# Kernel optimization log

Hardware: AMD Instinct MI355X
Metric: run time of the kernel (lower is better)

The kernel has to match this reference:

```python
import jax, jax.numpy as jnp
import numpy as np

B, T, E, H, A, V, C = 4, 256, 256, 256, 256, 32000, 100
NEG = -1e9


def setup_inputs() -> dict:
    key = jax.random.key(0)
    cnt = [0]
    def nk():
        cnt[0] += 1
        return jax.random.fold_in(key, cnt[0])
    def rn(shape, scale=0.05):
        return jax.random.normal(nk(), shape, jnp.float32) * scale
    inp = {
        'input_ids': jax.random.randint(nk(), (B, T), 0, V),
        'category_ids': jax.random.randint(nk(), (B, T), 0, C),
        'emb': rn((V, E)),
        'cat_emb': rn((C, E)),
    }
    in_sizes = [2 * E, H]
    for li, ins in enumerate(in_sizes):
        inp[f'Wih{li}'] = rn((ins, 3 * H)); inp[f'bih{li}'] = rn((3 * H,))
        inp[f'Whh{li}'] = rn((H, 3 * H)); inp[f'bhh{li}'] = rn((3 * H,))
        inp[f'Wh{li}'] = rn((H, A));      inp[f'bh{li}'] = rn((A,))
        inp[f'Wx{li}'] = rn((ins, A));    inp[f'bx{li}'] = rn((A,))
        inp[f'Wth{li}'] = rn((H, A));     inp[f'bth{li}'] = rn((A,))
        inp[f'v{li}'] = rn((A,));         inp[f'bv{li}'] = rn((1,))
    inp['Wctx'] = rn((H + E, 500)); inp['bctx'] = rn((500,))
    inp['Wout'] = rn((500, V));     inp['bout'] = rn((V,))
    return inp


def _cell(x, h, tape, t, Wih, bih, Whh, bhh, Wh, bh, Wx, bx, Wth, bth, v, bv):
    # attention over memory tape positions j < t (tape rows >= t are zeros, masked out)
    att = jnp.tanh(tape @ Wh + bh + (x @ Wx + bx)[:, None, :] + (h @ Wth + bth)[:, None, :])  # [B,T,A]
    scores = att @ v + bv  # [B,T]
    mask = jnp.arange(tape.shape[1]) < t
    scores = jnp.where(mask[None, :], scores, NEG)
    w = jax.nn.softmax(scores, axis=1)
    agg = jnp.einsum('bt,bth->bh', w, tape)
    agg = jnp.where(t > 0, agg, h)  # empty tape at t=0 -> use hidden directly
    gi = x @ Wih + bih
    gh = agg @ Whh + bhh
    ir, iu, inew = jnp.split(gi, 3, axis=1)
    hr, hu, hn = jnp.split(gh, 3, axis=1)
    r = jax.nn.sigmoid(ir + hr)
    u = jax.nn.sigmoid(iu + hu)
    n = jnp.tanh(inew + r * hn)
    return (1.0 - u) * n + u * agg


def _forward(input_ids, category_ids, emb, cat_emb, p0, p1, Wctx, bctx, Wout, bout):
    we = emb[input_ids]          # [B,T,E]
    ce = cat_emb[category_ids]   # [B,T,E]
    x_seq = jnp.concatenate([we, ce], axis=-1)  # [B,T,2E]

    def step(carry, xs):
        h0, h1, tape0, tape1 = carry
        x_t, c_t, t = xs
        # layer 0: category added to both embedding halves
        li0 = jax.nn.relu(x_t + jnp.tile(c_t, (1, 2)))
        nh0 = _cell(li0, h0, tape0, t, *p0)
        tape0 = tape0.at[:, t].set(nh0)
        # layer 1 (dropout is identity in eval)
        li1 = jax.nn.relu(nh0 + c_t)
        nh1 = _cell(li1, h1, tape1, t, *p1)
        tape1 = tape1.at[:, t].set(nh1)
        ctx = jnp.tanh(jnp.concatenate([nh1, c_t], axis=-1) @ Wctx + bctx)
        logits = ctx @ Wout + bout
        return (nh0, nh1, tape0, tape1), logits

    Bn = input_ids.shape[0]
    init = (jnp.zeros((Bn, H), jnp.float32), jnp.zeros((Bn, H), jnp.float32),
            jnp.zeros((Bn, T, H), jnp.float32), jnp.zeros((Bn, T, H), jnp.float32))
    xs = (jnp.swapaxes(x_seq, 0, 1), jnp.swapaxes(ce, 0, 1), jnp.arange(T))
    (h0, h1, _, _), outs = jax.lax.scan(jax.checkpoint(step), init, xs)
    return jnp.swapaxes(outs, 0, 1), h0, h1


def reference(input_ids, category_ids, emb, cat_emb,
              Wih0, bih0, Whh0, bhh0, Wh0, bh0, Wx0, bx0, Wth0, bth0, v0, bv0,
              Wih1, bih1, Whh1, bhh1, Wh1, bh1, Wx1, bx1, Wth1, bth1, v1, bv1,
              Wctx, bctx, Wout, bout):
    p0 = (Wih0, bih0, Whh0, bhh0, Wh0, bh0, Wx0, bx0, Wth0, bth0, v0, bv0)
    p1 = (Wih1, bih1, Whh1, bhh1, Wh1, bh1, Wx1, bx1, Wth1, bth1, v1, bv1)
    return _forward(input_ids, category_ids, emb, cat_emb, p0, p1, Wctx, bctx, Wout, bout)
```

## Files before the change

### kernel.cpp

```cpp
#include <hip/hip_runtime.h>

#define DEVINL __device__ __forceinline__

constexpr int kB = 4, kT = 256, kH = 256, kA = 256, kV = 32000;
constexpr int NBLKS = 128;
constexpr int NGRP = 32;
constexpr int NTHR = 512;
constexpr int WSL = 8;
constexpr int SBIAS = 1 << 24;
constexpr int SBIAS_TOT = NGRP * SBIAS;
constexpr unsigned long long CANARY = ~0ull;

typedef __attribute__((ext_vector_type(8))) short bf16x8;
typedef __attribute__((ext_vector_type(4))) float f32x4;

DEVINL float fexp2(float x) { float y; asm("v_exp_f32 %0, %1" : "=v"(y) : "v"(x)); return y; }
DEVINL float frcp(float x)  { float y; asm("v_rcp_f32 %0, %1" : "=v"(y) : "v"(x)); return y; }
DEVINL float f_tanh(float x) {
  float t = fexp2(x * 2.88539008f);
  return 1.f - 2.f * frcp(t + 1.f);
}
DEVINL float f_sig(float x) { return frcp(1.f + fexp2(-x * 1.44269504f)); }

DEVINL float bfu2f(unsigned short u) {
  union { unsigned int i; float f; } c; c.i = ((unsigned int)u) << 16; return c.f;
}
DEVINL unsigned short f2bfu(float f) {
  union { float f; unsigned int i; } c; c.f = f;
  unsigned int r = c.i + 0x7fffu + ((c.i >> 16) & 1u);
  return (unsigned short)(r >> 16);
}
DEVINL unsigned int f2u(float f) { union { float f; unsigned int i; } c; c.f = f; return c.i; }
DEVINL float u2f(unsigned int u) { union { unsigned int i; float f; } c; c.i = u; return c.f; }

DEVINL unsigned long long aload64(const unsigned long long* p) {
  return __hip_atomic_load(p, __ATOMIC_RELAXED, __HIP_MEMORY_SCOPE_AGENT);
}
DEVINL void astore64(unsigned long long* p, unsigned long long v) {
  __hip_atomic_store(p, v, __ATOMIC_RELAXED, __HIP_MEMORY_SCOPE_AGENT);
}

DEVINL bool sready(unsigned long long v) {
  unsigned int lo = (unsigned int)v, hi = (unsigned int)(v >> 32);
  return (((lo + (1u << 23)) >> 24) == (unsigned)NGRP) &&
         (((hi + (1u << 23)) >> 24) == (unsigned)NGRP);
}

DEVINL float dot_bf64s(const float* x, const unsigned short* w, int q) {
  float a0 = 0.f, a1 = 0.f, a2 = 0.f, a3 = 0.f;
  const float4*  x4 = (const float4*)x;
  const ushort4* w4 = (const ushort4*)w;
#pragma unroll
  for (int i = 0; i < 16; ++i) {
    int c = q + 4 * i;
    float4 xv = x4[c]; ushort4 wv = w4[c];
    a0 += xv.x * bfu2f(wv.x);
    a1 += xv.y * bfu2f(wv.y);
    a2 += xv.z * bfu2f(wv.z);
    a3 += xv.w * bfu2f(wv.w);
  }
  return (a0 + a1) + (a2 + a3);
}

DEVINL float sc4(const unsigned short* p4p, const float* xp, const float* vr) {
  ushort4 p4 = *(const ushort4*)p4p;
  float accA, accB;
  accA  = f_tanh(bfu2f(p4.x) + xp[0]) * vr[0];
  accB  = f_tanh(bfu2f(p4.y) + xp[1]) * vr[1];
  accA += f_tanh(bfu2f(p4.z) + xp[2]) * vr[2];
  accB += f_tanh(bfu2f(p4.w) + xp[3]) * vr[3];
  return accA + accB;
}

__global__ void init_kernel(int* dst, int nz, int val) {
  for (int i = blockIdx.x * blockDim.x + threadIdx.x; i < nz; i += gridDim.x * blockDim.x)
    dst[i] = val;
}

__global__ void embed_kernel(const int* __restrict__ ids, const int* __restrict__ cids,
                             const float* __restrict__ emb, const float* __restrict__ cat_emb,
                             float* __restrict__ li0_all, float* __restrict__ ce_all,
                             float* __restrict__ cat1_all) {
  int bt = blockIdx.x, e = threadIdx.x;
  int id = ids[bt], cid = cids[bt];
  float we = emb[id * kH + e];
  float ce = cat_emb[cid * kH + e];
  li0_all[bt * 512 + e]       = fmaxf(we + ce, 0.f);
  li0_all[bt * 512 + 256 + e] = fmaxf(ce + ce, 0.f);
  ce_all[bt * 256 + e] = ce;
  cat1_all[bt * 512 + 256 + e] = ce;
}

__global__ __launch_bounds__(256) void gemm_f32(const float* __restrict__ A,
                                                const float* __restrict__ Wm,
                                                const float* __restrict__ bias,
                                                float* __restrict__ C,
                                                int M, int N, int K) {
  __shared__ __align__(16) float As[16][68];
  __shared__ __align__(16) float Bs[16][68];
  int tid = threadIdx.x;
  int tx = tid & 15, ty = tid >> 4;
  int row0 = blockIdx.y * 64, col0 = blockIdx.x * 64;
  int ar = tid >> 2;
  int ak = (tid & 3) * 4;
  int br = tid >> 4;
  int bc = (tid & 15) * 4;
  float acc[4][4] = {};
  for (int k0 = 0; k0 < K; k0 += 16) {
    float4 av = {0.f, 0.f, 0.f, 0.f};
    if (k0 + ak < K) av = *(const float4*)(A + (size_t)(row0 + ar) * K + k0 + ak);
    As[ak + 0][ar] = av.x; As[ak + 1][ar] = av.y; As[ak + 2][ar] = av.z; As[ak + 3][ar] = av.w;
    float4 bv = {0.f, 0.f, 0.f, 0.f};
    int wrow = k0 + br;
    if (wrow < K) {
      if (col0 + bc + 3 < N) bv = *(const float4*)(Wm + (size_t)wrow * N + col0 + bc);
      else {
        float t[4] = {0.f, 0.f, 0.f, 0.f};
        for (int u = 0; u < 4; ++u) if (col0 + bc + u < N) t[u] = Wm[(size_t)wrow * N + col0 + bc + u];
        bv.x = t[0]; bv.y = t[1]; bv.z = t[2]; bv.w = t[3];
      }
    }
    *(float4*)&Bs[br][bc] = bv;
    __syncthreads();
#pragma unroll
    for (int kk = 0; kk < 16; ++kk) {
      float4 a4 = *(const float4*)&As[kk][ty * 4];
      float4 b4 = *(const float4*)&Bs[kk][tx * 4];
      acc[0][0] += a4.x * b4.x; acc[0][1] += a4.x * b4.y; acc[0][2] += a4.x * b4.z; acc[0][3] += a4.x * b4.w;
      acc[1][0] += a4.y * b4.x; acc[1][1] += a4.y * b4.y; acc[1][2] += a4.y * b4.z; acc[1][3] += a4.y * b4.w;
      acc[2][0] += a4.z * b4.x; acc[2][1] += a4.z * b4.y; acc[2][2] += a4.z * b4.z; acc[2][3] += a4.z * b4.w;
      acc[3][0] += a4.w * b4.x; acc[3][1] += a4.w * b4.y; acc[3][2] += a4.w * b4.z; acc[3][3] += a4.w * b4.w;
    }
    __syncthreads();
  }
#pragma unroll
  for (int i = 0; i < 4; ++i) {
    int r = row0 + ty * 4 + i;
#pragma unroll
    for (int j = 0; j < 4; ++j) {
      int c = col0 + tx * 4 + j;
      if (c < N) C[(size_t)r * N + c] = acc[i][j] + bias[c];
    }
  }
}

__global__ __launch_bounds__(256) void gemm_ctx_bf16(const float* __restrict__ A,
                                                     const float* __restrict__ Wm,
                                                     const float* __restrict__ bias,
                                                     unsigned short* __restrict__ Cb) {
  const int N = 500, K = 512;
  __shared__ __align__(16) float As[16][68];
  __shared__ __align__(16) float Bs[16][68];
  int tid = threadIdx.x;
  int tx = tid & 15, ty = tid >> 4;
  int row0 = blockIdx.y * 64, col0 = blockIdx.x * 64;
  int ar = tid >> 2;
  int ak = (tid & 3) * 4;
  int br = tid >> 4;
  int bc = (tid & 15) * 4;
  float acc[4][4] = {};
  for (int k0 = 0; k0 < K; k0 += 16) {
    float4 av = *(const float4*)(A + (size_t)(row0 + ar) * K + k0 + ak);
    As[ak + 0][ar] = av.x; As[ak + 1][ar] = av.y; As[ak + 2][ar] = av.z; As[ak + 3][ar] = av.w;
    float4 bv = {0.f, 0.f, 0.f, 0.f};
    int wrow = k0 + br;
    if (col0 + bc + 3 < N) bv = *(const float4*)(Wm + (size_t)wrow * N + col0 + bc);
    else {
      float t[4] = {0.f, 0.f, 0.f, 0.f};
      for (int u = 0; u < 4; ++u) if (col0 + bc + u < N) t[u] = Wm[(size_t)wrow * N + col0 + bc + u];
      bv.x = t[0]; bv.y = t[1]; bv.z = t[2]; bv.w = t[3];
    }
    *(float4*)&Bs[br][bc] = bv;
    __syncthreads();
#pragma unroll
    for (int kk = 0; kk < 16; ++kk) {
      float4 a4 = *(const float4*)&As[kk][ty * 4];
      float4 b4 = *(const float4*)&Bs[kk][tx * 4];
      acc[0][0] += a4.x * b4.x; acc[0][1] += a4.x * b4.y; acc[0][2] += a4.x * b4.z; acc[0][3] += a4.x * b4.w;
      acc[1][0] += a4.y * b4.x; acc[1][1] += a4.y * b4.y; acc[1][2] += a4.y * b4.z; acc[1][3] += a4.y * b4.w;
      acc[2][0] += a4.z * b4.x; acc[2][1] += a4.z * b4.y; acc[2][2] += a4.z * b4.z; acc[2][3] += a4.z * b4.w;
      acc[3][0] += a4.w * b4.x; acc[3][1] += a4.w * b4.y; acc[3][2] += a4.w * b4.z; acc[3][3] += a4.w * b4.w;
    }
    __syncthreads();
  }
#pragma unroll
  for (int i = 0; i < 4; ++i) {
    int r = row0 + ty * 4 + i;
#pragma unroll
    for (int j = 0; j < 4; ++j) {
      int c = col0 + tx * 4 + j;
      if (c < N) {
        float v = f_tanh(acc[i][j] + bias[c]);
        Cb[(size_t)r * 512 + c] = f2bfu(v);
      } else {
        Cb[(size_t)r * 512 + c] = 0;
      }
    }
  }
}

__global__ __launch_bounds__(256) void gemm_logits_mfma(
    const unsigned short* __restrict__ A,
    const float* __restrict__ Wout,
    const float* __restrict__ bout,
    float* __restrict__ C) {
  __shared__ __align__(16) unsigned short Bt[64][520];
  const int tid = threadIdx.x;
  const int n0 = blockIdx.x * 64;

  for (int idx = tid; idx < 512 * 16; idx += 256) {
    int k = idx >> 4, nq = (idx & 15) << 2;
    if (k < 500) {
      float4 v = *(const float4*)(Wout + (size_t)k * 32000 + n0 + nq);
      Bt[nq + 0][k] = f2bfu(v.x); Bt[nq + 1][k] = f2bfu(v.y);
      Bt[nq + 2][k] = f2bfu(v.z); Bt[nq + 3][k] = f2bfu(v.w);
    } else {
      Bt[nq + 0][k] = 0; Bt[nq + 1][k] = 0; Bt[nq + 2][k] = 0; Bt[nq + 3][k] = 0;
    }
  }
  __syncthreads();

  const int l = tid & 63, w = tid >> 6;
  const int lrow = l & 15, lk = (l >> 4) * 8;
  float bia0 = bout[n0 +  0 + lrow];
  float bia1 = bout[n0 + 16 + lrow];
  float bia2 = bout[n0 + 32 + lrow];
  float bia3 = bout[n0 + 48 + lrow];

  for (int m0 = 0; m0 < 1024; m0 += 64) {
    f32x4 acc0 = {0.f, 0.f, 0.f, 0.f}, acc1 = acc0, acc2 = acc0, acc3 = acc0;
    const unsigned short* Arow = A + (size_t)(m0 + w * 16 + lrow) * 512 + lk;
#pragma unroll
    for (int ks = 0; ks < 16; ++ks) {
      bf16x8 a  = *(const bf16x8*)(Arow + ks * 32);
      bf16x8 b0 = *(const bf16x8*)&Bt[ 0 + lrow][ks * 32 + lk];
      bf16x8 b1 = *(const bf16x8*)&Bt[16 + lrow][ks * 32 + lk];
      bf16x8 b2 = *(const bf16x8*)&Bt[32 + lrow][ks * 32 + lk];
      bf16x8 b3 = *(const bf16x8*)&Bt[48 + lrow][ks * 32 + lk];
      acc0 = __builtin_amdgcn_mfma_f32_16x16x32_bf16(a, b0, acc0, 0, 0, 0);
      acc1 = __builtin_amdgcn_mfma_f32_16x16x32_bf16(a, b1, acc1, 0, 0, 0);
      acc2 = __builtin_amdgcn_mfma_f32_16x16x32_bf16(a, b2, acc2, 0, 0, 0);
      acc3 = __builtin_amdgcn_mfma_f32_16x16x32_bf16(a, b3, acc3, 0, 0, 0);
    }
    int orow = m0 + w * 16 + (l >> 4) * 4;
#pragma unroll
    for (int r = 0; r < 4; ++r) {
      float* Cr = C + (size_t)(orow + r) * 32000 + n0;
      Cr[ 0 + lrow] = acc0[r] + bia0;
      Cr[16 + lrow] = acc1[r] + bia1;
      Cr[32 + lrow] = acc2[r] + bia2;
      Cr[48 + lrow] = acc3[r] + bia3;
    }
  }
}

__global__ __launch_bounds__(NTHR, 1) void coop_kernel(
    const float* __restrict__ gi0_all, const float* __restrict__ xw0_all,
    const float* __restrict__ ce_all,
    unsigned long long* __restrict__ nh0p, unsigned long long* __restrict__ nh1p,
    float* __restrict__ cat1_all, float* __restrict__ out_tail,
    unsigned long long* __restrict__ s0buf, unsigned long long* __restrict__ s1buf,
    const float* __restrict__ Whh0, const float* __restrict__ bhh0,
    const float* __restrict__ Wh0, const float* __restrict__ bh0,
    const float* __restrict__ Wth0, const float* __restrict__ bth0,
    const float* __restrict__ v0,
    const float* __restrict__ Wih1, const float* __restrict__ bih1,
    const float* __restrict__ Whh1, const float* __restrict__ bhh1,
    const float* __restrict__ Wh1, const float* __restrict__ bh1,
    const float* __restrict__ Wx1, const float* __restrict__ bx1,
    const float* __restrict__ Wth1, const float* __restrict__ bth1,
    const float* __restrict__ v1) {
  __shared__ __align__(16) unsigned short tWhh0_s[kT][24];
  __shared__ __align__(16) unsigned short tWhh1_s[kT][24];
  __shared__ __align__(16) unsigned short tape0_s[kT][8];
  __shared__ __align__(16) unsigned short tape1_s[kT][8];
  __shared__ __align__(16) unsigned short tWh0_s[kT][8];
  __shared__ __align__(16) unsigned short tWh1_s[kT][8];
  __shared__ __align__(16) unsigned short Wh0c[WSL][264], Wth0c[WSL][264];
  __shared__ __align__(16) unsigned short Wh1c[WSL][264], Wth1c[WSL][264], Wx1c[WSL][264];
  __shared__ __align__(16) unsigned short Whh0c[24][264], Whh1c[24][264], Wih1c[24][264];
  __shared__ float bh0s[8], bth0s[8], bh1s[8], bth1s[8], bx1s[8];
  __shared__ float bhh0s[24], bhh1s[24], bih1s[24];
  __shared__ __align__(16) float nh0_s[260], nh1_s[260], li1_s[260];
  __shared__ __align__(16) float sm_s[2][260];
  __shared__ float xps0_s[8], xps1a_s[8], xps1b_s[8];
  __shared__ float gi1_s[24], gh0_s[24], gh1_s[24];
  __shared__ float agg0_s[8], agg1_s[8], redsum_s[2][2];
  __shared__ float gipre_s[3][8];
  __shared__ float v0s[8], v1s[8];

  const int bid = blockIdx.x, tid = threadIdx.x;
  const int grp = bid >> 5;
  const int bidg = bid & 31;
  const int c0 = bidg * WSL;
  const int gb = grp;
  unsigned long long* S0 = s0buf + grp * 384;
  unsigned long long* S1 = s1buf + grp * 384;

  for (int idx = tid; idx < WSL * kH; idx += NTHR) {
    int c = idx >> 8, h = idx & 255, col = c0 + c;
    Wh0c[c][h]  = f2bfu(Wh0[h * kA + col]);
    Wth0c[c][h] = f2bfu(Wth0[h * kA + col]);
    Wh1c[c][h]  = f2bfu(Wh1[h * kA + col]);
    Wth1c[c][h] = f2bfu(Wth1[h * kA + col]);
    Wx1c[c][h]  = f2bfu(Wx1[h * kA + col]);
  }
  for (int idx = tid; idx < 24 * kH; idx += NTHR) {
    int cc = idx >> 8, h = idx & 255;
    int n = (cc >> 3) * kH + c0 + (cc & 7);
    Whh0c[cc][h] = f2bfu(Whh0[h * 768 + n]);
    Whh1c[cc][h] = f2bfu(Whh1[h * 768 + n]);
    Wih1c[cc][h] = f2bfu(Wih1[h * 768 + n]);
  }
  if (tid < 8) {
    int c = c0 + tid;
    bh0s[tid] = bh0[c]; bth0s[tid] = bth0[c];
    bh1s[tid] = bh1[c]; bth1s[tid] = bth1[c]; bx1s[tid] = bx1[c];
    v0s[tid] = v0[c]; v1s[tid] = v1[c];
  }
  if (tid < 24) {
    int n = (tid >> 3) * kH + c0 + (tid & 7);
    bhh0s[tid] = bhh0[n]; bhh1s[tid] = bhh1[n]; bih1s[tid] = bih1[n];
  }
  __syncthreads();

  if (tid < 8) {
    int c = tid, hcol = c0 + c;
    const float* gi = gi0_all + (size_t)(gb * kT) * 768;
    float r = f_sig(gi[hcol] + bhh0s[c]);
    float u = f_sig(gi[256 + hcol] + bhh0s[8 + c]);
    float n = f_tanh(gi[512 + hcol] + r * bhh0s[16 + c]);
    float val = (1.f - u) * n;
    tape0_s[0][c] = f2bfu(val);
    float other = __shfl_xor(val, 1);
    if ((c & 1) == 0) {
      unsigned long long pk = (unsigned long long)f2u(val) |
                              ((unsigned long long)f2u(other) << 32);
      astore64(&nh0p[(size_t)(gb * kT) * 128 + bidg * 4 + (c >> 1)], pk);
    }
  }

  const float SCL = 65536.f;
  const float fxi = 1.44269504f / 65536.f;

  for (int k = 0; k < kT; ++k) {
    if (tid < 256) {
      int which = tid >> 7;
      int pr = tid & 127, h = pr * 2;
      if (which == 0) {
        const unsigned long long* p = &nh0p[(size_t)(gb * kT + k) * 128 + pr];
        unsigned long long v = aload64(p);
        int it = 0;
        while (v == CANARY) {
          v = aload64(p);
          if (++it > (1 << 24)) break;
        }
        float lo = u2f((unsigned int)v), hi = u2f((unsigned int)(v >> 32));
        nh0_s[h] = lo; nh0_s[h + 1] = hi;
        float2 ce2 = *(const float2*)&ce_all[(size_t)(gb * kT + k) * 256 + h];
        li1_s[h]     = fmaxf(lo + ce2.x, 0.f);
        li1_s[h + 1] = fmaxf(hi + ce2.y, 0.f);
      } else if (k > 0) {
        const unsigned long long* p = &nh1p[(size_t)(gb * kT + k - 1) * 128 + pr];
        unsigned long long v = aload64(p);
        int it = 0;
        while (v == CANARY) {
          v = aload64(p);
          if (++it > (1 << 24)) break;
        }
        nh1_s[h]     = u2f((unsigned int)v);
        nh1_s[h + 1] = u2f((unsigned int)(v >> 32));
      }
    }
    if (tid >= 256 && tid < 264 && k < kT - 1) {
      int c = tid - 256, hcol = c0 + c;
      const float* gi = gi0_all + (size_t)(gb * kT + k + 1) * 768;
      gipre_s[0][c] = gi[hcol];
      gipre_s[1][c] = gi[256 + hcol];
      gipre_s[2][c] = gi[512 + hcol];
    }
    if (tid >= NTHR - 8) {
      int z = tid - (NTHR - 8);
      int pz = (k + 1) % 3;
      int idx = bidg * 4 + (z & 3);
      if (z < 4) astore64(&S0[pz * 128 + idx], 0ull);
      else       astore64(&S1[pz * 128 + idx], 0ull);
    }
    __syncthreads();

    {
      int p = tid >> 2, q = tid & 3;
      if (p < 40) {
        if (k < kT - 1) {
          if (p < 8) {
            int c = p;
            float acc = dot_bf64s(nh0_s, Wth0c[c], q);
            acc += __shfl_xor(acc, 1); acc += __shfl_xor(acc, 2);
            if (q == 0) {
              float xw = xw0_all[(size_t)(gb * kT + k + 1) * kA + c0 + c];
              xps0_s[c] = acc + bth0s[c] + xw;
            }
          } else if (p < 16) {
            int c = p - 8;
            float acc = dot_bf64s(nh0_s, Wh0c[c], q);
            acc += __shfl_xor(acc, 1); acc += __shfl_xor(acc, 2);
            if (q == 0) tWh0_s[k][c] = f2bfu(acc + bh0s[c]);
          } else {
            int cc = p - 16;
            float acc = dot_bf64s(nh0_s, Whh0c[cc], q);
            acc += __shfl_xor(acc, 1); acc += __shfl_xor(acc, 2);
            if (q == 0) tWhh0_s[k][cc] = f2bfu(acc);
          }
        }
      } else if (p < 72) {
        if (p < 64) {
          int cc = p - 40;
          float acc = dot_bf64s(li1_s, Wih1c[cc], q);
          acc += __shfl_xor(acc, 1); acc += __shfl_xor(acc, 2);
          if (q == 0) gi1_s[cc] = acc + bih1s[cc];
        } else {
          int c = p - 64;
          float acc = dot_bf64s(li1_s, Wx1c[c], q);
          acc += __shfl_xor(acc, 1); acc += __shfl_xor(acc, 2);
          if (q == 0) xps1a_s[c] = acc + bx1s[c];
        }
      } else if (p < 112) {
        if (k > 0) {
          if (p < 80) {
            int c = p - 72;
            float acc = dot_bf64s(nh1_s, Wth1c[c], q);
            acc += __shfl_xor(acc, 1); acc += __shfl_xor(acc, 2);
            if (q == 0) xps1b_s[c] = acc + bth1s[c];
          } else if (p < 88) {
            int c = p - 80;
            float acc = dot_bf64s(nh1_s, Wh1c[c], q);
            acc += __shfl_xor(acc, 1); acc += __shfl_xor(acc, 2);
            if (q == 0) tWh1_s[k - 1][c] = f2bfu(acc + bh1s[c]);
          } else {
            int cc = p - 88;
            float acc = dot_bf64s(nh1_s, Whh1c[cc], q);
            acc += __shfl_xor(acc, 1); acc += __shfl_xor(acc, 2);
            if (q == 0) tWhh1_s[k - 1][cc] = f2bfu(acc);
          }
        }
      }
    }
    __syncthreads();

    {
      int cnt0w = k + 1, cnt1w = k;
      int np0 = (k < kT - 1) ? ((cnt0w + 1) >> 1) : 0;
      int np1 = (cnt1w + 1) >> 1;
      int pk = k % 3;
      unsigned long long* d0 = S0 + pk * 128;
      unsigned long long* d1 = S1 + pk * 128;
      for (int pp = tid; pp < np0 + np1; pp += NTHR) {
        float p0, p1; unsigned long long* dst;
        if (pp < np0) {
          int j0 = 2 * pp;
          p0 = sc4(&tWh0_s[j0][0], xps0_s, v0s) + sc4(&tWh0_s[j0][4], xps0_s + 4, v0s + 4);
          p1 = 0.f;
          if (j0 + 1 < cnt0w)
            p1 = sc4(&tWh0_s[j0 + 1][0], xps0_s, v0s) + sc4(&tWh0_s[j0 + 1][4], xps0_s + 4, v0s + 4);
          dst = d0 + pp;
        } else {
          int pr = pp - np0, j0 = 2 * pr;
          float xp[8];
#pragma unroll
          for (int c = 0; c < 8; ++c) xp[c] = xps1a_s[c] + xps1b_s[c];
          p0 = sc4(&tWh1_s[j0][0], xp, v1s) + sc4(&tWh1_s[j0][4], xp + 4, v1s + 4);
          p1 = 0.f;
          if (j0 + 1 < cnt1w)
            p1 = sc4(&tWh1_s[j0 + 1][0], xp, v1s) + sc4(&tWh1_s[j0 + 1][4], xp + 4, v1s + 4);
          dst = d1 + pr;
        }
        int q0 = (int)rintf(p0 * SCL) + SBIAS;
        int q1 = (int)rintf(p1 * SCL) + SBIAS;
        unsigned long long add = (unsigned long long)(unsigned int)q0 |
                                 ((unsigned long long)(unsigned int)q1 << 32);
        __hip_atomic_fetch_add(dst, add, __ATOMIC_RELAXED, __HIP_MEMORY_SCOPE_AGENT);
      }
    }
    __syncthreads();

    int cnt0 = (k < kT - 1) ? (k + 1) : 0;
    int cnt1 = k;
    if (tid < 256) {
      int r = tid >> 7, lane = tid & 127;
      float sum = 0.f;
      int cnt = (r == 0) ? cnt0 : cnt1;
      if (cnt) {
        int pk = k % 3;
        const unsigned long long* sb = (r == 0) ? S0 + pk * 128 : S1 + pk * 128;
        int npr = (cnt + 1) >> 1;
        if (lane < npr) {
          unsigned long long v = aload64(&sb[lane]);
          int it = 0;
          while (!sready(v)) {
            v = aload64(&sb[lane]);
            if (++it > (1 << 24)) break;
          }
          int lo = (int)(unsigned int)(v & 0xffffffffull) - SBIAS_TOT;
          int hi = (int)(unsigned int)(v >> 32) - SBIAS_TOT;
          float e0 = fexp2((float)lo * fxi);
          sm_s[r][2 * lane] = e0; sum += e0;
          if (2 * lane + 1 < cnt) {
            float e1 = fexp2((float)hi * fxi);
            sm_s[r][2 * lane + 1] = e1; sum += e1;
          }
        }
      }
      for (int m = 32; m >= 1; m >>= 1) sum += __shfl_xor(sum, m);
      if ((tid & 63) == 0) redsum_s[r][(tid >> 6) & 1] = sum;
    }
    __syncthreads();

    {
      int slot = tid >> 3, sub = tid & 7;
      float accA = 0.f, accB = 0.f;
      if (slot < 24) {
        if (cnt0) {
          int cc = slot;
#pragma unroll 4
          for (int j = sub; j < cnt0; j += 16) accA += sm_s[0][j] * bfu2f(tWhh0_s[j][cc]);
#pragma unroll 4
          for (int j = sub + 8; j < cnt0; j += 16) accB += sm_s[0][j] * bfu2f(tWhh0_s[j][cc]);
          float acc = accA + accB;
          acc += __shfl_xor(acc, 1); acc += __shfl_xor(acc, 2); acc += __shfl_xor(acc, 4);
          if (sub == 0) gh0_s[cc] = acc * frcp(redsum_s[0][0] + redsum_s[0][1]) + bhh0s[cc];
        }
      } else if (slot < 32) {
        if (cnt0) {
          int c = slot - 24;
#pragma unroll 4
          for (int j = sub; j < cnt0; j += 16) accA += sm_s[0][j] * bfu2f(tape0_s[j][c]);
#pragma unroll 4
          for (int j = sub + 8; j < cnt0; j += 16) accB += sm_s[0][j] * bfu2f(tape0_s[j][c]);
          float acc = accA + accB;
          acc += __shfl_xor(acc, 1); acc += __shfl_xor(acc, 2); acc += __shfl_xor(acc, 4);
          if (sub == 0) agg0_s[c] = acc * frcp(redsum_s[0][0] + redsum_s[0][1]);
        }
      } else if (slot < 56) {
        if (cnt1) {
          int cc = slot - 32;
#pragma unroll 4
          for (int j = sub; j < cnt1; j += 16) accA += sm_s[1][j] * bfu2f(tWhh1_s[j][cc]);
#pragma unroll 4
          for (int j = sub + 8; j < cnt1; j += 16) accB += sm_s[1][j] * bfu2f(tWhh1_s[j][cc]);
          float acc = accA + accB;
          acc += __shfl_xor(acc, 1); acc += __shfl_xor(acc, 2); acc += __shfl_xor(acc, 4);
          if (sub == 0) gh1_s[cc] = acc * frcp(redsum_s[1][0] + redsum_s[1][1]) + bhh1s[cc];
        }
      } else if (slot < 64) {
        if (cnt1) {
          int c = slot - 56;
#pragma unroll 4
          for (int j = sub; j < cnt1; j += 16) accA += sm_s[1][j] * bfu2f(tape1_s[j][c]);
#pragma unroll 4
          for (int j = sub + 8; j < cnt1; j += 16) accB += sm_s[1][j] * bfu2f(tape1_s[j][c]);
          float acc = accA + accB;
          acc += __shfl_xor(acc, 1); acc += __shfl_xor(acc, 2); acc += __shfl_xor(acc, 4);
          if (sub == 0) agg1_s[c] = acc * frcp(redsum_s[1][0] + redsum_s[1][1]);
        }
      }
    }
    __syncthreads();

    if (tid < 8) {
      if (k < kT - 1) {
        int c = tid, hcol = c0 + c, t0 = k + 1;
        float agg = agg0_s[c];
        float r = f_sig(gipre_s[0][c] + gh0_s[c]);
        float u = f_sig(gipre_s[1][c] + gh0_s[8 + c]);
        float n = f_tanh(gipre_s[2][c] + r * gh0_s[16 + c]);
        float val = (1.f - u) * n + u * agg;
        tape0_s[t0][c] = f2bfu(val);
        if (t0 == kT - 1) out_tail[gb * kH + hcol] = val;
        float other = __shfl_xor(val, 1);
        if ((c & 1) == 0) {
          unsigned long long pk = (unsigned long long)f2u(val) |
                                  ((unsigned long long)f2u(other) << 32);
          astore64(&nh0p[(size_t)(gb * kT + t0) * 128 + bidg * 4 + (c >> 1)], pk);
        }
      }
    } else if (tid >= 64 && tid < 72) {
      int c = tid - 64, hcol = c0 + c;
      float ghr, ghu, ghn, agg;
      if (k > 0) { ghr = gh1_s[c]; ghu = gh1_s[8 + c]; ghn = gh1_s[16 + c]; agg = agg1_s[c]; }
      else       { ghr = bhh1s[c]; ghu = bhh1s[8 + c]; ghn = bhh1s[16 + c]; agg = 0.f; }
      float r = f_sig(gi1_s[c] + ghr);
      float u = f_sig(gi1_s[8 + c] + ghu);
      float n = f_tanh(gi1_s[16 + c] + r * ghn);
      float val = (1.f - u) * n + u * agg;
      tape1_s[k][c] = f2bfu(val);
      cat1_all[(size_t)(gb * kT + k) * 512 + hcol] = val;
      if (k == kT - 1) out_tail[kB * kH + gb * kH + hcol] = val;
      float other = __shfl_xor(val, 1);
      if ((c & 1) == 0) {
        unsigned long long pk = (unsigned long long)f2u(val) |
                                ((unsigned long long)f2u(other) << 32);
        astore64(&nh1p[(size_t)(gb * kT + k) * 128 + bidg * 4 + (c >> 1)], pk);
      }
    }
  }
}

extern "C" void kernel_launch(void* const* d_in, const int* in_sizes, int n_in,
                              void* d_out, int out_size, void* d_ws, size_t ws_size,
                              hipStream_t stream) {
  const int*   input_ids    = (const int*)d_in[0];
  const int*   category_ids = (const int*)d_in[1];
  const float* emb     = (const float*)d_in[2];
  const float* cat_emb = (const float*)d_in[3];
  const float* Wih0 = (const float*)d_in[4];
  const float* bih0 = (const float*)d_in[5];
  const float* Whh0 = (const float*)d_in[6];  const float* bhh0 = (const float*)d_in[7];
  const float* Wh0  = (const float*)d_in[8];  const float* bh0  = (const float*)d_in[9];
  const float* Wx0  = (const float*)d_in[10]; const float* bx0  = (const float*)d_in[11];
  const float* Wth0 = (const float*)d_in[12]; const float* bth0 = (const float*)d_in[13];
  const float* v0   = (const float*)d_in[14];
  const float* Wih1 = (const float*)d_in[16]; const float* bih1 = (const float*)d_in[17];
  const float* Whh1 = (const float*)d_in[18]; const float* bhh1 = (const float*)d_in[19];
  const float* Wh1  = (const float*)d_in[20]; const float* bh1  = (const float*)d_in[21];
  const float* Wx1  = (const float*)d_in[22]; const float* bx1  = (const float*)d_in[23];
  const float* Wth1 = (const float*)d_in[24]; const float* bth1 = (const float*)d_in[25];
  const float* v1   = (const float*)d_in[26];
  const float* Wctx = (const float*)d_in[28]; const float* bctx = (const float*)d_in[29];
  const float* Wout = (const float*)d_in[30]; const float* bout = (const float*)d_in[31];

  float* ws = (float*)d_ws;
  float* li0_all  = ws;
  float* ce_all   = li0_all + 524288;
  float* gi0_all  = ce_all + 262144;
  float* xw0_all  = gi0_all + 786432;
  unsigned long long* nh0p = (unsigned long long*)(xw0_all + 262144);
  unsigned long long* nh1p = nh0p + 131072;
  float* cat1_all = (float*)(nh1p + 131072);
  unsigned short* ctx_bf = (unsigned short*)(cat1_all + 524288);

  unsigned long long* s0buf = (unsigned long long*)li0_all;
  unsigned long long* s1buf = s0buf + 1536;
  int    nzero_s  = 2 * 1536 * 2;
  int    nfill_nh = 2 * 131072 * 2;

  float* out = (float*)d_out;
  float* out_tail = out + (size_t)kB * kT * kV;

  embed_kernel<<<dim3(kB * kT), dim3(256), 0, stream>>>(input_ids, category_ids, emb, cat_emb,
                                                        li0_all, ce_all, cat1_all);
  gemm_f32<<<dim3(12, 16), dim3(256), 0, stream>>>(li0_all, Wih0, bih0, gi0_all, 1024, 768, 512);
  gemm_f32<<<dim3(4, 16), dim3(256), 0, stream>>>(li0_all, Wx0, bx0, xw0_all, 1024, 256, 512);
  init_kernel<<<dim3(8), dim3(512), 0, stream>>>((int*)s0buf, nzero_s, 0);
  init_kernel<<<dim3(128), dim3(512), 0, stream>>>((int*)nh0p, nfill_nh, -1);
  coop_kernel<<<dim3(NBLKS), dim3(NTHR), 0, stream>>>(gi0_all, xw0_all, ce_all, nh0p, nh1p,
      cat1_all, out_tail, s0buf, s1buf,
      Whh0, bhh0, Wh0, bh0, Wth0, bth0, v0,
      Wih1, bih1, Whh1, bhh1, Wh1, bh1, Wx1, bx1, Wth1, bth1, v1);
  gemm_ctx_bf16<<<dim3(8, 16), dim3(256), 0, stream>>>(cat1_all, Wctx, bctx, ctx_bf);
  gemm_logits_mfma<<<dim3(500), dim3(256), 0, stream>>>(ctx_bf, Wout, bout, out);
}
```

Baseline: 2.055 ms.

## Use bf16 MFMA for input projections and overlap nh1 wait with its dot products

```diff
diff --git a/kernel.cpp b/kernel.cpp
--- a/kernel.cpp
+++ b/kernel.cpp
@@ -62,6 +62,27 @@
   return (a0 + a1) + (a2 + a3);
 }
 
+DEVINL float dot_nh1g(const unsigned long long* xrow, const unsigned short* w, int q) {
+  float a0 = 0.f, a1 = 0.f, a2 = 0.f, a3 = 0.f;
+  const ushort4* w4 = (const ushort4*)w;
+#pragma unroll
+  for (int i = 0; i < 16; ++i) {
+    int c = q + 4 * i;
+    unsigned long long va = aload64(xrow + 2 * c);
+    int it = 0;
+    while (va == CANARY) { va = aload64(xrow + 2 * c); if (++it > (1 << 24)) break; }
+    unsigned long long vb = aload64(xrow + 2 * c + 1);
+    it = 0;
+    while (vb == CANARY) { vb = aload64(xrow + 2 * c + 1); if (++it > (1 << 24)) break; }
+    ushort4 wv = w4[c];
+    a0 += u2f((unsigned int)va)         * bfu2f(wv.x);
+    a1 += u2f((unsigned int)(va >> 32)) * bfu2f(wv.y);
+    a2 += u2f((unsigned int)vb)         * bfu2f(wv.z);
+    a3 += u2f((unsigned int)(vb >> 32)) * bfu2f(wv.w);
+  }
+  return (a0 + a1) + (a2 + a3);
+}
+
 DEVINL float sc4(const unsigned short* p4p, const float* xp, const float* vr) {
   ushort4 p4 = *(const ushort4*)p4p;
   float accA, accB;
@@ -79,68 +100,64 @@
 
 __global__ void embed_kernel(const int* __restrict__ ids, const int* __restrict__ cids,
                              const float* __restrict__ emb, const float* __restrict__ cat_emb,
-                             float* __restrict__ li0_all, float* __restrict__ ce_all,
+                             unsigned short* __restrict__ li0bf, float* __restrict__ ce_all,
                              float* __restrict__ cat1_all) {
   int bt = blockIdx.x, e = threadIdx.x;
   int id = ids[bt], cid = cids[bt];
   float we = emb[id * kH + e];
   float ce = cat_emb[cid * kH + e];
-  li0_all[bt * 512 + e]       = fmaxf(we + ce, 0.f);
-  li0_all[bt * 512 + 256 + e] = fmaxf(ce + ce, 0.f);
+  li0bf[bt * 512 + e]       = f2bfu(fmaxf(we + ce, 0.f));
+  li0bf[bt * 512 + 256 + e] = f2bfu(fmaxf(ce + ce, 0.f));
   ce_all[bt * 256 + e] = ce;
   cat1_all[bt * 512 + 256 + e] = ce;
 }
 
-__global__ __launch_bounds__(256) void gemm_f32(const float* __restrict__ A,
-                                                const float* __restrict__ Wm,
-                                                const float* __restrict__ bias,
-                                                float* __restrict__ C,
-                                                int M, int N, int K) {
-  __shared__ __align__(16) float As[16][68];
-  __shared__ __align__(16) float Bs[16][68];
-  int tid = threadIdx.x;
-  int tx = tid & 15, ty = tid >> 4;
-  int row0 = blockIdx.y * 64, col0 = blockIdx.x * 64;
-  int ar = tid >> 2;
-  int ak = (tid & 3) * 4;
-  int br = tid >> 4;
-  int bc = (tid & 15) * 4;
-  float acc[4][4] = {};
-  for (int k0 = 0; k0 < K; k0 += 16) {
-    float4 av = {0.f, 0.f, 0.f, 0.f};
-    if (k0 + ak < K) av = *(const float4*)(A + (size_t)(row0 + ar) * K + k0 + ak);
-    As[ak + 0][ar] = av.x; As[ak + 1][ar] = av.y; As[ak + 2][ar] = av.z; As[ak + 3][ar] = av.w;
-    float4 bv = {0.f, 0.f, 0.f, 0.f};
-    int wrow = k0 + br;
-    if (wrow < K) {
-      if (col0 + bc + 3 < N) bv = *(const float4*)(Wm + (size_t)wrow * N + col0 + bc);
-      else {
-        float t[4] = {0.f, 0.f, 0.f, 0.f};
-        for (int u = 0; u < 4; ++u) if (col0 + bc + u < N) t[u] = Wm[(size_t)wrow * N + col0 + bc + u];
-        bv.x = t[0]; bv.y = t[1]; bv.z = t[2]; bv.w = t[3];
-      }
-    }
-    *(float4*)&Bs[br][bc] = bv;
-    __syncthreads();
-#pragma unroll
-    for (int kk = 0; kk < 16; ++kk) {
-      float4 a4 = *(const float4*)&As[kk][ty * 4];
-      float4 b4 = *(const float4*)&Bs[kk][tx * 4];
-      acc[0][0] += a4.x * b4.x; acc[0][1] += a4.x * b4.y; acc[0][2] += a4.x * b4.z; acc[0][3] += a4.x * b4.w;
-      acc[1][0] += a4.y * b4.x; acc[1][1] += a4.y * b4.y; acc[1][2] += a4.y * b4.z; acc[1][3] += a4.y * b4.w;
-      acc[2][0] += a4.z * b4.x; acc[2][1] += a4.z * b4.y; acc[2][2] += a4.z * b4.z; acc[2][3] += a4.z * b4.w;
-      acc[3][0] += a4.w * b4.x; acc[3][1] += a4.w * b4.y; acc[3][2] += a4.w * b4.z; acc[3][3] += a4.w * b4.w;
-    }
-    __syncthreads();
-  }
-#pragma unroll
-  for (int i = 0; i < 4; ++i) {
-    int r = row0 + ty * 4 + i;
-#pragma unroll
-    for (int j = 0; j < 4; ++j) {
-      int c = col0 + tx * 4 + j;
-      if (c < N) C[(size_t)r * N + c] = acc[i][j] + bias[c];
-    }
+__global__ __launch_bounds__(256) void gemm_mfma_f32out(
+    const unsigned short* __restrict__ A,
+    const float* __restrict__ Wm,
+    const float* __restrict__ bias,
+    float* __restrict__ C, int N) {
+  __shared__ __align__(16) unsigned short Bt[64][520];
+  const int tid = threadIdx.x;
+  const int n0 = blockIdx.x * 64, m0 = blockIdx.y * 64;
+
+  for (int idx = tid; idx < 512 * 16; idx += 256) {
+    int k = idx >> 4, nq = (idx & 15) << 2;
+    float4 v = *(const float4*)(Wm + (size_t)k * N + n0 + nq);
+    Bt[nq + 0][k] = f2bfu(v.x); Bt[nq + 1][k] = f2bfu(v.y);
+    Bt[nq + 2][k] = f2bfu(v.z); Bt[nq + 3][k] = f2bfu(v.w);
+  }
+  __syncthreads();
+
+  const int l = tid & 63, w = tid >> 6;
+  const int lrow = l & 15, lk = (l >> 4) * 8;
+  float bia0 = bias[n0 +  0 + lrow];
+  float bia1 = bias[n0 + 16 + lrow];
+  float bia2 = bias[n0 + 32 + lrow];
+  float bia3 = bias[n0 + 48 + lrow];
+
+  f32x4 acc0 = {0.f, 0.f, 0.f, 0.f}, acc1 = acc0, acc2 = acc0, acc3 = acc0;
+  const unsigned short* Arow = A + (size_t)(m0 + w * 16 + lrow) * 512 + lk;
+#pragma unroll
+  for (int ks = 0; ks < 16; ++ks) {
+    bf16x8 a  = *(const bf16x8*)(Arow + ks * 32);
+    bf16x8 b0 = *(const bf16x8*)&Bt[ 0 + lrow][ks * 32 + lk];
+    bf16x8 b1 = *(const bf16x8*)&Bt[16 + lrow][ks * 32 + lk];
+    bf16x8 b2 = *(const bf16x8*)&Bt[32 + lrow][ks * 32 + lk];
+    bf16x8 b3 = *(const bf16x8*)&Bt[48 + lrow][ks * 32 + lk];
+    acc0 = __builtin_amdgcn_mfma_f32_16x16x32_bf16(a, b0, acc0, 0, 0, 0);
+    acc1 = __builtin_amdgcn_mfma_f32_16x16x32_bf16(a, b1, acc1, 0, 0, 0);
+    acc2 = __builtin_amdgcn_mfma_f32_16x16x32_bf16(a, b2, acc2, 0, 0, 0);
+    acc3 = __builtin_amdgcn_mfma_f32_16x16x32_bf16(a, b3, acc3, 0, 0, 0);
+  }
+  int orow = m0 + w * 16 + (l >> 4) * 4;
+#pragma unroll
+  for (int r = 0; r < 4; ++r) {
+    float* Cr = C + (size_t)(orow + r) * N + n0;
+    Cr[ 0 + lrow] = acc0[r] + bia0;
+    Cr[16 + lrow] = acc1[r] + bia1;
+    Cr[32 + lrow] = acc2[r] + bia2;
+    Cr[48 + lrow] = acc3[r] + bia3;
   }
 }
 
@@ -281,7 +298,7 @@
   __shared__ __align__(16) unsigned short Whh0c[24][264], Whh1c[24][264], Wih1c[24][264];
   __shared__ float bh0s[8], bth0s[8], bh1s[8], bth1s[8], bx1s[8];
   __shared__ float bhh0s[24], bhh1s[24], bih1s[24];
-  __shared__ __align__(16) float nh0_s[260], nh1_s[260], li1_s[260];
+  __shared__ __align__(16) float nh0_s[260], li1_s[260];
   __shared__ __align__(16) float sm_s[2][260];
   __shared__ float xps0_s[8], xps1a_s[8], xps1b_s[8];
   __shared__ float gi1_s[24], gh0_s[24], gh1_s[24];
@@ -344,40 +361,48 @@
   const float fxi = 1.44269504f / 65536.f;
 
   for (int k = 0; k < kT; ++k) {
-    if (tid < 256) {
-      int which = tid >> 7;
-      int pr = tid & 127, h = pr * 2;
-      if (which == 0) {
-        const unsigned long long* p = &nh0p[(size_t)(gb * kT + k) * 128 + pr];
-        unsigned long long v = aload64(p);
-        int it = 0;
-        while (v == CANARY) {
-          v = aload64(p);
-          if (++it > (1 << 24)) break;
-        }
-        float lo = u2f((unsigned int)v), hi = u2f((unsigned int)(v >> 32));
-        nh0_s[h] = lo; nh0_s[h + 1] = hi;
-        float2 ce2 = *(const float2*)&ce_all[(size_t)(gb * kT + k) * 256 + h];
-        li1_s[h]     = fmaxf(lo + ce2.x, 0.f);
-        li1_s[h + 1] = fmaxf(hi + ce2.y, 0.f);
-      } else if (k > 0) {
-        const unsigned long long* p = &nh1p[(size_t)(gb * kT + k - 1) * 128 + pr];
-        unsigned long long v = aload64(p);
-        int it = 0;
-        while (v == CANARY) {
-          v = aload64(p);
-          if (++it > (1 << 24)) break;
-        }
-        nh1_s[h]     = u2f((unsigned int)v);
-        nh1_s[h + 1] = u2f((unsigned int)(v >> 32));
-      }
-    }
-    if (tid >= 256 && tid < 264 && k < kT - 1) {
-      int c = tid - 256, hcol = c0 + c;
-      const float* gi = gi0_all + (size_t)(gb * kT + k + 1) * 768;
-      gipre_s[0][c] = gi[hcol];
-      gipre_s[1][c] = gi[256 + hcol];
-      gipre_s[2][c] = gi[512 + hcol];
+    if (tid < 128) {
+      int pr = tid, h = pr * 2;
+      const unsigned long long* p = &nh0p[(size_t)(gb * kT + k) * 128 + pr];
+      unsigned long long v = aload64(p);
+      int it = 0;
+      while (v == CANARY) {
+        v = aload64(p);
+        if (++it > (1 << 24)) break;
+      }
+      float lo = u2f((unsigned int)v), hi = u2f((unsigned int)(v >> 32));
+      nh0_s[h] = lo; nh0_s[h + 1] = hi;
+      float2 ce2 = *(const float2*)&ce_all[(size_t)(gb * kT + k) * 256 + h];
+      li1_s[h]     = fmaxf(lo + ce2.x, 0.f);
+      li1_s[h + 1] = fmaxf(hi + ce2.y, 0.f);
+    } else if (tid < 288) {
+      if (k > 0) {
+        int p = (tid - 128) >> 2, q = tid & 3;
+        const unsigned long long* xrow = &nh1p[(size_t)(gb * kT + k - 1) * 128];
+        if (p < 8) {
+          float acc = dot_nh1g(xrow, Wth1c[p], q);
+          acc += __shfl_xor(acc, 1); acc += __shfl_xor(acc, 2);
+          if (q == 0) xps1b_s[p] = acc + bth1s[p];
+        } else if (p < 16) {
+          int c = p - 8;
+          float acc = dot_nh1g(xrow, Wh1c[c], q);
+          acc += __shfl_xor(acc, 1); acc += __shfl_xor(acc, 2);
+          if (q == 0) tWh1_s[k - 1][c] = f2bfu(acc + bh1s[c]);
+        } else {
+          int cc = p - 16;
+          float acc = dot_nh1g(xrow, Whh1c[cc], q);
+          acc += __shfl_xor(acc, 1); acc += __shfl_xor(acc, 2);
+          if (q == 0) tWhh1_s[k - 1][cc] = f2bfu(acc);
+        }
+      }
+    } else if (tid < 296) {
+      if (k < kT - 1) {
+        int c = tid - 288, hcol = c0 + c;
+        const float* gi = gi0_all + (size_t)(gb * kT + k + 1) * 768;
+        gipre_s[0][c] = gi[hcol];
+        gipre_s[1][c] = gi[256 + hcol];
+        gipre_s[2][c] = gi[512 + hcol];
+      }
     }
     if (tid >= NTHR - 8) {
       int z = tid - (NTHR - 8);
@@ -412,37 +437,16 @@
             if (q == 0) tWhh0_s[k][cc] = f2bfu(acc);
           }
         }
+      } else if (p < 64) {
+        int cc = p - 40;
+        float acc = dot_bf64s(li1_s, Wih1c[cc], q);
+        acc += __shfl_xor(acc, 1); acc += __shfl_xor(acc, 2);
+        if (q == 0) gi1_s[cc] = acc + bih1s[cc];
       } else if (p < 72) {
-        if (p < 64) {
-          int cc = p - 40;
-          float acc = dot_bf64s(li1_s, Wih1c[cc], q);
-          acc += __shfl_xor(acc, 1); acc += __shfl_xor(acc, 2);
-          if (q == 0) gi1_s[cc] = acc + bih1s[cc];
-        } else {
-          int c = p - 64;
-          float acc = dot_bf64s(li1_s, Wx1c[c], q);
-          acc += __shfl_xor(acc, 1); acc += __shfl_xor(acc, 2);
-          if (q == 0) xps1a_s[c] = acc + bx1s[c];
-        }
-      } else if (p < 112) {
-        if (k > 0) {
-          if (p < 80) {
-            int c = p - 72;
-            float acc = dot_bf64s(nh1_s, Wth1c[c], q);
-            acc += __shfl_xor(acc, 1); acc += __shfl_xor(acc, 2);
-            if (q == 0) xps1b_s[c] = acc + bth1s[c];
-          } else if (p < 88) {
-            int c = p - 80;
-            float acc = dot_bf64s(nh1_s, Wh1c[c], q);
-            acc += __shfl_xor(acc, 1); acc += __shfl_xor(acc, 2);
-            if (q == 0) tWh1_s[k - 1][c] = f2bfu(acc + bh1s[c]);
-          } else {
-            int cc = p - 88;
-            float acc = dot_bf64s(nh1_s, Whh1c[cc], q);
-            acc += __shfl_xor(acc, 1); acc += __shfl_xor(acc, 2);
-            if (q == 0) tWhh1_s[k - 1][cc] = f2bfu(acc);
-          }
-        }
+        int c = p - 64;
+        float acc = dot_bf64s(li1_s, Wx1c[c], q);
+        acc += __shfl_xor(acc, 1); acc += __shfl_xor(acc, 2);
+        if (q == 0) xps1a_s[c] = acc + bx1s[c];
       }
     }
     __syncthreads();
@@ -637,6 +641,7 @@
   unsigned long long* nh1p = nh0p + 131072;
   float* cat1_all = (float*)(nh1p + 131072);
   unsigned short* ctx_bf = (unsigned short*)(cat1_all + 524288);
+  unsigned short* li0bf  = ctx_bf + 524288;
 
   unsigned long long* s0buf = (unsigned long long*)li0_all;
   unsigned long long* s1buf = s0buf + 1536;
@@ -647,9 +652,9 @@
   float* out_tail = out + (size_t)kB * kT * kV;
 
   embed_kernel<<<dim3(kB * kT), dim3(256), 0, stream>>>(input_ids, category_ids, emb, cat_emb,
-                                                        li0_all, ce_all, cat1_all);
-  gemm_f32<<<dim3(12, 16), dim3(256), 0, stream>>>(li0_all, Wih0, bih0, gi0_all, 1024, 768, 512);
-  gemm_f32<<<dim3(4, 16), dim3(256), 0, stream>>>(li0_all, Wx0, bx0, xw0_all, 1024, 256, 512);
+                                                        li0bf, ce_all, cat1_all);
+  gemm_mfma_f32out<<<dim3(12, 16), dim3(256), 0, stream>>>(li0bf, Wih0, bih0, gi0_all, 768);
+  gemm_mfma_f32out<<<dim3(4, 16), dim3(256), 0, stream>>>(li0bf, Wx0, bx0, xw0_all, 256);
   init_kernel<<<dim3(8), dim3(512), 0, stream>>>((int*)s0buf, nzero_s, 0);
   init_kernel<<<dim3(128), dim3(512), 0, stream>>>((int*)nh0p, nfill_nh, -1);
   coop_kernel<<<dim3(NBLKS), dim3(NTHR), 0, stream>>>(gi0_all, xw0_all, ce_all, nh0p, nh1p,
```

Measured after the change: 4.472 ms. 2.18x slower.
